# Kernel optimization log

Measured on AMD Instinct MI355X. Metric: run time of the kernel, lower is better.

## Reference

```python
import jax, jax.numpy as jnp
import numpy as np

B, N, M, J, D, PF = 4, 131072, 10475, 55, 64, 486


def setup_inputs() -> dict:
    key = jax.random.key(0)
    ks = jax.random.split(key, 16)
    return {
        "pts": jax.random.normal(ks[0], (B, N, 3), jnp.float32),
        "betas": jax.random.normal(ks[1], (B, 10), jnp.float32),
        "pose_feature": jax.random.normal(ks[2], (B, PF), jnp.float32),
        "init_spdir": jax.random.normal(ks[3], (M, 3, 10), jnp.float32),
        "init_podir": jax.random.normal(ks[4], (PF, 3 * M), jnp.float32),
        "init_faces": jax.random.randint(ks[5], (N, 3), 0, M, jnp.int32),
        "tfs_A": jax.random.normal(ks[6], (B, J, 4, 4), jnp.float32),
        "tfs_inv": jax.random.normal(ks[7], (1, J, 4, 4), jnp.float32),
        "poseoff_cano": jax.random.normal(ks[8], (1, N, 3), jnp.float32),
        "lbsw": jax.random.uniform(ks[9], (1, N, J), jnp.float32),
        "lbs_voxel": jax.random.uniform(ks[10], (1, J, D, D, D), jnp.float32),
        "vox_scale": jnp.ones((1, 1, 3), jnp.float32),
        "vox_offset": jnp.zeros((1, 1, 3), jnp.float32),
        "mask": jax.random.randint(ks[11], (B, N), 0, 2, jnp.int32),
    }


def _trilinear(vox, x, scale, offset):
    # vox: [J,D,D,D], x: [b,n,3] -> [b,n,J] trilinearly interpolated weights
    nj, nd = vox.shape[0], vox.shape[-1]
    g = jnp.clip(x * scale + offset, -1.0, 1.0)          # normalized coords
    t = (g + 1.0) * 0.5 * (nd - 1)                        # voxel coords
    i0 = jnp.clip(jnp.floor(t), 0, nd - 2).astype(jnp.int32)
    f = t - i0                                            # fractional part
    vf = vox.reshape(nj, -1)                              # [J, D^3]
    out = jnp.zeros(x.shape[:-1] + (nj,), x.dtype)
    for dx in (0, 1):
        for dy in (0, 1):
            for dz in (0, 1):
                ix = i0[..., 0] + dx
                iy = i0[..., 1] + dy
                iz = i0[..., 2] + dz
                wgt = ((f[..., 0] if dx else 1.0 - f[..., 0]) *
                       (f[..., 1] if dy else 1.0 - f[..., 1]) *
                       (f[..., 2] if dz else 1.0 - f[..., 2]))
                fid = (ix * nd + iy) * nd + iz            # flat voxel index [b,n]
                out = out + wgt[..., None] * jnp.moveaxis(vf[:, fid], 0, -1)
    return out


def reference(pts, betas, pose_feature, init_spdir, init_podir, init_faces,
              tfs_A, tfs_inv, poseoff_cano, lbsw, lbs_voxel, vox_scale,
              vox_offset, mask):
    b, n, _ = pts.shape
    # blend-shape offsets on template vertices
    shape_full = jnp.einsum('bl,mkl->bmk', betas, init_spdir)      # [b,M,3]
    pose_full = (pose_feature @ init_podir).reshape(b, -1, 3)      # [b,M,3]
    # face-vertex gather then average over the 3 vertices of each face
    shape_off = shape_full[:, init_faces].mean(axis=2)             # [b,F,3]
    pose_off = pose_full[:, init_faces].mean(axis=2)               # [b,F,3]
    x = pts + shape_off + pose_off - poseoff_cano                  # canonical pts + offsets
    # voxel-grid skinning-weight lookup at canonical points
    w_vox = _trilinear(lbs_voxel[0], pts, vox_scale, vox_offset)   # [b,n,J]
    w = jnp.where(mask[..., None] > 0, lbsw, w_vox)
    w = w / jnp.clip(w.sum(-1, keepdims=True), 1e-8)
    # per-point blended transforms: A @ A_inv_template
    tfs = tfs_A @ tfs_inv                                          # [b,J,4,4]
    T = jnp.einsum('bnj,bjrc->bnrc', w, tfs)                       # [b,n,4,4]
    xh = jnp.concatenate([x, jnp.ones_like(x[..., :1])], axis=-1)
    posed = jnp.einsum('bnrc,bnc->bnr', T, xh)[..., :3]
    return posed.reshape(b, n, 1, 3), T
```

## Files before the change

kernel.cpp:

```cpp
#include <hip/hip_runtime.h>

#define B_  4
#define N_  131072
#define J_  55
#define JP_ 56
#define D_  64
#define D3_ 262144
#define PF_ 486
#define COLS_ 31425

#define GZ_ 4096
#define OZ_ 123

#define BL16(u) __uint_as_float((u) << 16)
#define BH16(u) __uint_as_float((u) & 0xffff0000u)

typedef float f4a __attribute__((ext_vector_type(4), aligned(4)));

__device__ __forceinline__ unsigned short f2bf(float v) {
    unsigned u = __float_as_uint(v);
    u += 0x7fffu + ((u >> 16) & 1u);
    return (unsigned short)(u >> 16);
}

__global__ __launch_bounds__(256) void k_tfs(const float* __restrict__ A,
                                             const float* __restrict__ Ainv,
                                             float* __restrict__ tfsP) {
    int tid = blockIdx.x * 256 + threadIdx.x;
    if (tid >= B_ * JP_ * 16) return;
    int rc = tid & 15;
    int jb = tid >> 4;
    int j = jb % JP_;
    int b = jb / JP_;
    float v = 0.f;
    if (j < J_) {
        int r = rc >> 2, c = rc & 3;
#pragma unroll
        for (int k = 0; k < 4; ++k)
            v += A[((b * J_ + j) * 4 + r) * 4 + k] * Ainv[(j * 4 + k) * 4 + c];
    }
    tfsP[tid] = v;
}

__global__ __launch_bounds__(256) void k_prelude(
    const float* __restrict__ vox, const float* __restrict__ tfsP,
    uint4* __restrict__ Gtb, float* __restrict__ Stb,
    const float* __restrict__ pf, const float* __restrict__ podir,
    const float* __restrict__ betas, const float* __restrict__ spdir,
    float* __restrict__ off_full) {
    int bx = blockIdx.x;
    int tid = threadIdx.x;

    if (bx < GZ_) {
        int b = (bx & 7) >> 1;
        int chunk = ((bx >> 3) << 1) | (bx & 1);
        int v = chunk * 256 + tid;
        float g[16];
#pragma unroll
        for (int r = 0; r < 16; ++r) g[r] = 0.f;
        float s = 0.f;
        const float* tb = tfsP + b * (JP_ * 16);
        float wa[11], wb[11];
#pragma unroll
        for (int k = 0; k < 11; ++k) wa[k] = vox[(size_t)k * D3_ + v];
        for (int j0 = 0; j0 < J_; j0 += 11) {
            if (j0 + 11 < J_) {
#pragma unroll
                for (int k = 0; k < 11; ++k)
                    wb[k] = vox[(size_t)(j0 + 11 + k) * D3_ + v];
            }
#pragma unroll
            for (int k = 0; k < 11; ++k) {
                float w = wa[k];
                s += w;
                const float* tr = tb + (j0 + k) * 16;
#pragma unroll
                for (int r = 0; r < 16; ++r) g[r] += w * tr[r];
            }
#pragma unroll
            for (int k = 0; k < 11; ++k) wa[k] = wb[k];
        }
        if (b == 0) Stb[v] = s;
        unsigned gw[8];
#pragma unroll
        for (int k = 0; k < 8; ++k)
            gw[k] = (unsigned)f2bf(g[2 * k]) |
                    ((unsigned)f2bf(g[2 * k + 1]) << 16);
        uint4* gp = Gtb + ((size_t)b * D3_ + v) * 2;
        gp[0] = make_uint4(gw[0], gw[1], gw[2], gw[3]);
        gp[1] = make_uint4(gw[4], gw[5], gw[6], gw[7]);
    } else {
        int col = (bx - GZ_) * 256 + tid;
        if (col >= COLS_) return;
        float a0 = 0.f, a1 = 0.f, a2 = 0.f, a3 = 0.f;
        {
            float sp[10];
#pragma unroll
            for (int l = 0; l < 10; ++l) sp[l] = spdir[col * 10 + l];
#pragma unroll
            for (int l = 0; l < 10; ++l) {
                a0 += betas[0 * 10 + l] * sp[l];
                a1 += betas[1 * 10 + l] * sp[l];
                a2 += betas[2 * 10 + l] * sp[l];
                a3 += betas[3 * 10 + l] * sp[l];
            }
        }
        int p = 0;
        for (; p + 16 <= PF_; p += 16) {
            float v16[16];
#pragma unroll
            for (int k = 0; k < 16; ++k)
                v16[k] = podir[(size_t)(p + k) * COLS_ + col];
#pragma unroll
            for (int k = 0; k < 16; ++k) {
                a0 += pf[0 * PF_ + p + k] * v16[k];
                a1 += pf[1 * PF_ + p + k] * v16[k];
                a2 += pf[2 * PF_ + p + k] * v16[k];
                a3 += pf[3 * PF_ + p + k] * v16[k];
            }
        }
        for (; p < PF_; ++p) {
            float v = podir[(size_t)p * COLS_ + col];
            a0 += pf[0 * PF_ + p] * v;
            a1 += pf[1 * PF_ + p] * v;
            a2 += pf[2 * PF_ + p] * v;
            a3 += pf[3 * PF_ + p] * v;
        }
        off_full[0 * COLS_ + col] = a0;
        off_full[1 * COLS_ + col] = a1;
        off_full[2 * COLS_ + col] = a2;
        off_full[3 * COLS_ + col] = a3;
    }
}

#define ACC8(Toff, qa, qb)                                 \
    T[Toff + 0] += w0 * BL16(qa.x) + w1 * BL16(qb.x);      \
    T[Toff + 1] += w0 * BH16(qa.x) + w1 * BH16(qb.x);      \
    T[Toff + 2] += w0 * BL16(qa.y) + w1 * BL16(qb.y);      \
    T[Toff + 3] += w0 * BH16(qa.y) + w1 * BH16(qb.y);      \
    T[Toff + 4] += w0 * BL16(qa.z) + w1 * BL16(qb.z);      \
    T[Toff + 5] += w0 * BH16(qa.z) + w1 * BH16(qb.z);      \
    T[Toff + 6] += w0 * BL16(qa.w) + w1 * BL16(qb.w);      \
    T[Toff + 7] += w0 * BH16(qa.w) + w1 * BH16(qb.w);

__global__ __launch_bounds__(256) void k_main(
    const float* __restrict__ pts, const int* __restrict__ faces,
    const float* __restrict__ poseoff, const int* __restrict__ mask,
    const float* __restrict__ vox_scale, const float* __restrict__ vox_offset,
    const float* __restrict__ off_full, const float* __restrict__ tfsP,
    const float* __restrict__ lbsw, const uint4* __restrict__ Gtb,
    const float* __restrict__ Stb,
    float* __restrict__ out_posed, float* __restrict__ out_T) {
    __shared__ float sx0[256], sx1[256], sx2[256];
    __shared__ float sf0[256], sf1[256], sf2[256];
    __shared__ int   scell[256];
    __shared__ unsigned short lst[256];
    __shared__ int wc[4];

    int bid = blockIdx.x;
    int b  = (bid & 7) >> 1;
    int nc = ((bid >> 3) << 1) | (bid & 1);
    int tid = threadIdx.x;
    int n = nc * 256 + tid;
    int i = (b << 17) | n;

    float px = pts[3 * i + 0], py = pts[3 * i + 1], pz = pts[3 * i + 2];
    int f0 = faces[3 * n + 0], f1 = faces[3 * n + 1], f2 = faces[3 * n + 2];
    const float* ob = off_full + b * COLS_;
    const float c3 = 1.f / 3.f;
    float ox = (ob[f0 * 3 + 0] + ob[f1 * 3 + 0] + ob[f2 * 3 + 0]) * c3;
    float oy = (ob[f0 * 3 + 1] + ob[f1 * 3 + 1] + ob[f2 * 3 + 1]) * c3;
    float oz = (ob[f0 * 3 + 2] + ob[f1 * 3 + 2] + ob[f2 * 3 + 2]) * c3;
    sx0[tid] = px + ox - poseoff[3 * n + 0];
    sx1[tid] = py + oy - poseoff[3 * n + 1];
    sx2[tid] = pz + oz - poseoff[3 * n + 2];

    bool isv = !(mask[i] > 0);
    if (isv) {
        float sxc = vox_scale[0], syc = vox_scale[1], szc = vox_scale[2];
        float o0 = vox_offset[0], o1 = vox_offset[1], o2 = vox_offset[2];
        float gx = fminf(fmaxf(px * sxc + o0, -1.f), 1.f);
        float gy = fminf(fmaxf(py * syc + o1, -1.f), 1.f);
        float gz = fminf(fmaxf(pz * szc + o2, -1.f), 1.f);
        float tx = (gx + 1.f) * 0.5f * (D_ - 1);
        float ty = (gy + 1.f) * 0.5f * (D_ - 1);
        float tz = (gz + 1.f) * 0.5f * (D_ - 1);
        int ix = (int)floorf(tx); if (ix > D_ - 2) ix = D_ - 2; if (ix < 0) ix = 0;
        int iy = (int)floorf(ty); if (iy > D_ - 2) iy = D_ - 2; if (iy < 0) iy = 0;
        int iz = (int)floorf(tz); if (iz > D_ - 2) iz = D_ - 2; if (iz < 0) iz = 0;
        sf0[tid] = tx - ix;
        sf1[tid] = ty - iy;
        sf2[tid] = tz - iz;
        scell[tid] = (ix * D_ + iy) * D_ + iz;
    }

    unsigned long long bal = __ballot(isv);
    int lane = tid & 63, wid = tid >> 6;
    if (lane == 0) wc[wid] = __popcll(bal);
    __syncthreads();
    int pre = 0;
#pragma unroll
    for (int k = 0; k < 4; ++k) pre += (k < wid) ? wc[k] : 0;
    int tot = wc[0] + wc[1] + wc[2] + wc[3];
    unsigned long long lt = ((unsigned long long)1 << lane) - 1ull;
    int vbefore = pre + __popcll(bal & lt);
    int pos = isv ? vbefore : (tot + (tid - vbefore));
    lst[pos] = (unsigned short)tid;
    __syncthreads();

    int slot = lst[tid];
    float x0 = sx0[slot], x1 = sx1[slot], x2 = sx2[slot];
    int ii = (b << 17) | (nc * 256 + slot);

    float T[16];
#pragma unroll
    for (int r = 0; r < 16; ++r) T[r] = 0.f;
    float wsum = 0.f;

    if (tid < tot) {
        float fx = sf0[slot], fy = sf1[slot], fz = sf2[slot];
        int cell = scell[slot];
        const uint4* Gb = Gtb + (size_t)b * D3_ * 2;
#pragma unroll
        for (int cc = 0; cc < 4; ++cc) {
            int fid = cell + ((cc & 2) ? D_ * D_ : 0) + ((cc & 1) ? D_ : 0);
            float wxy = ((cc & 2) ? fx : 1.f - fx) * ((cc & 1) ? fy : 1.f - fy);
            float w0 = wxy * (1.f - fz);
            float w1 = wxy * fz;
            const uint4* R = Gb + (size_t)fid * 2;
            uint4 q0 = R[0], q1 = R[1], q2 = R[2], q3 = R[3];
            wsum += w0 * Stb[fid] + w1 * Stb[fid + 1];
            ACC8(0, q0, q2)
            ACC8(8, q1, q3)
        }
    } else {
        int n2 = nc * 256 + slot;
        const float* lw = lbsw + (size_t)n2 * J_;
        f4a q[13];
#pragma unroll
        for (int k = 0; k < 13; ++k)
            q[k] = *(const f4a*)(lw + 4 * k);
        float w52 = lw[52], w53 = lw[53], w54 = lw[54];
        const float* tb = tfsP + b * (JP_ * 16);
#pragma unroll
        for (int k = 0; k < 13; ++k) {
#pragma unroll
            for (int m = 0; m < 4; ++m) {
                float w = q[k][m];
                wsum += w;
                const float* tr = tb + (k * 4 + m) * 16;
#pragma unroll
                for (int r = 0; r < 16; ++r) T[r] += w * tr[r];
            }
        }
        float wt[3] = { w52, w53, w54 };
#pragma unroll
        for (int m = 0; m < 3; ++m) {
            float w = wt[m];
            wsum += w;
            const float* tr = tb + (52 + m) * 16;
#pragma unroll
            for (int r = 0; r < 16; ++r) T[r] += w * tr[r];
        }
    }

    float inv = 1.f / fmaxf(wsum, 1e-8f);
    float t[16];
#pragma unroll
    for (int r = 0; r < 16; ++r) t[r] = T[r] * inv;
    out_posed[3 * ii + 0] = t[0] * x0 + t[1] * x1 + t[2] * x2 + t[3];
    out_posed[3 * ii + 1] = t[4] * x0 + t[5] * x1 + t[6] * x2 + t[7];
    out_posed[3 * ii + 2] = t[8] * x0 + t[9] * x1 + t[10] * x2 + t[11];
    float4* to = (float4*)(out_T + (size_t)ii * 16);
    to[0] = make_float4(t[0], t[1], t[2], t[3]);
    to[1] = make_float4(t[4], t[5], t[6], t[7]);
    to[2] = make_float4(t[8], t[9], t[10], t[11]);
    to[3] = make_float4(t[12], t[13], t[14], t[15]);
}

extern "C" void kernel_launch(void* const* d_in, const int* in_sizes, int n_in,
                              void* d_out, int out_size, void* d_ws, size_t ws_size,
                              hipStream_t stream) {
    const float* pts      = (const float*)d_in[0];
    const float* betas    = (const float*)d_in[1];
    const float* pf       = (const float*)d_in[2];
    const float* spdir    = (const float*)d_in[3];
    const float* podir    = (const float*)d_in[4];
    const int*   faces    = (const int*)d_in[5];
    const float* tfs_A    = (const float*)d_in[6];
    const float* tfs_inv  = (const float*)d_in[7];
    const float* poseoff  = (const float*)d_in[8];
    const float* lbsw     = (const float*)d_in[9];
    const float* vox      = (const float*)d_in[10];
    const float* vscale   = (const float*)d_in[11];
    const float* voffset  = (const float*)d_in[12];
    const int*   mask     = (const int*)d_in[13];

    char* w = (char*)d_ws;
    uint4* Gtb      = (uint4*)w;
    float* Stb      = (float*)(w + 33554432);
    float* off_full = (float*)(w + 34603008);
    float* tfsP     = (float*)(w + 35119104);

    float* out_posed = (float*)d_out;
    float* out_T     = out_posed + (size_t)B_ * N_ * 3;

    k_tfs<<<14, 256, 0, stream>>>(tfs_A, tfs_inv, tfsP);
    k_prelude<<<GZ_ + OZ_, 256, 0, stream>>>(
        vox, tfsP, Gtb, Stb, pf, podir, betas, spdir, off_full);
    k_main<<<2048, 256, 0, stream>>>(pts, faces, poseoff, mask, vscale,
                                     voffset, off_full, tfsP, lbsw, Gtb, Stb,
                                     out_posed, out_T);
}
```

Baseline: 293.7 us.

## Fold tfs computation into kernels and share voxel loads across batch pairs

Drops the separate k_tfs launch. Each block now computes the 55 blended A@A_inv transforms straight into shared memory. In the prelude, each block handles two batches for the same voxel chunk, so every voxel weight read from global memory feeds two 16-float accumulators, and the block count is halved. This roughly halves the prelude's dominant voxel-grid reads and removes one launch plus a workspace round trip. The cost is redundant per-block transform math, more register pressure from 32 accumulators, and extra shared memory in both kernels.

```diff
diff --git a/kernel.cpp b/kernel.cpp
--- a/kernel.cpp
+++ b/kernel.cpp
@@ -9,7 +9,7 @@
 #define PF_ 486
 #define COLS_ 31425
 
-#define GZ_ 4096
+#define GZ_ 2048
 #define OZ_ 123
 
 #define BL16(u) __uint_as_float((u) << 16)
@@ -23,27 +23,42 @@
     return (unsigned short)(u >> 16);
 }
 
-__global__ __launch_bounds__(256) void k_tfs(const float* __restrict__ A,
-                                             const float* __restrict__ Ainv,
-                                             float* __restrict__ tfsP) {
-    int tid = blockIdx.x * 256 + threadIdx.x;
-    if (tid >= B_ * JP_ * 16) return;
-    int rc = tid & 15;
-    int jb = tid >> 4;
-    int j = jb % JP_;
-    int b = jb / JP_;
-    float v = 0.f;
-    if (j < J_) {
-        int r = rc >> 2, c = rc & 3;
-#pragma unroll
-        for (int k = 0; k < 4; ++k)
-            v += A[((b * J_ + j) * 4 + r) * 4 + k] * Ainv[(j * 4 + k) * 4 + c];
+__device__ __forceinline__ void stage_tfs(int b, int tid,
+                                          const float* __restrict__ A,
+                                          const float* __restrict__ Ainv,
+                                          float* __restrict__ dst) {
+#pragma unroll
+    for (int base = 0; base < 896; base += 256) {
+        int idx = base + tid;
+        if (idx < 896) {
+            int j = idx >> 4, rc = idx & 15, r = rc >> 2, c = rc & 3;
+            float v = 0.f;
+            if (j < J_) {
+#pragma unroll
+                for (int k = 0; k < 4; ++k)
+                    v += A[((b * J_ + j) * 4 + r) * 4 + k] *
+                         Ainv[(j * 4 + k) * 4 + c];
+            }
+            dst[idx] = v;
+        }
     }
-    tfsP[tid] = v;
-}
+}
+
+#define GACC(gv, q)                                         \
+    {   float4 t0 = s4[(q) * 4 + 0], t1 = s4[(q) * 4 + 1],  \
+               t2 = s4[(q) * 4 + 2], t3 = s4[(q) * 4 + 3];  \
+        gv[0]  += w * t0.x; gv[1]  += w * t0.y;             \
+        gv[2]  += w * t0.z; gv[3]  += w * t0.w;             \
+        gv[4]  += w * t1.x; gv[5]  += w * t1.y;             \
+        gv[6]  += w * t1.z; gv[7]  += w * t1.w;             \
+        gv[8]  += w * t2.x; gv[9]  += w * t2.y;             \
+        gv[10] += w * t2.z; gv[11] += w * t2.w;             \
+        gv[12] += w * t3.x; gv[13] += w * t3.y;             \
+        gv[14] += w * t3.z; gv[15] += w * t3.w; }
 
 __global__ __launch_bounds__(256) void k_prelude(
-    const float* __restrict__ vox, const float* __restrict__ tfsP,
+    const float* __restrict__ A, const float* __restrict__ Ainv,
+    const float* __restrict__ vox,
     uint4* __restrict__ Gtb, float* __restrict__ Stb,
     const float* __restrict__ pf, const float* __restrict__ podir,
     const float* __restrict__ betas, const float* __restrict__ spdir,
@@ -52,14 +67,20 @@
     int tid = threadIdx.x;
 
     if (bx < GZ_) {
-        int b = (bx & 7) >> 1;
-        int chunk = ((bx >> 3) << 1) | (bx & 1);
+        __shared__ float stfs[2 * 896];
+        int bp = (bx & 4) >> 2;
+        int chunk = ((bx >> 3) << 2) | (bx & 3);
+        stage_tfs(2 * bp + 0, tid, A, Ainv, stfs);
+        stage_tfs(2 * bp + 1, tid, A, Ainv, stfs + 896);
+        __syncthreads();
+
         int v = chunk * 256 + tid;
-        float g[16];
-#pragma unroll
-        for (int r = 0; r < 16; ++r) g[r] = 0.f;
+        float g0[16], g1[16];
+#pragma unroll
+        for (int r = 0; r < 16; ++r) { g0[r] = 0.f; g1[r] = 0.f; }
         float s = 0.f;
-        const float* tb = tfsP + b * (JP_ * 16);
+        const float4* sa = (const float4*)stfs;
+        const float4* sb = (const float4*)(stfs + 896);
         float wa[11], wb[11];
 #pragma unroll
         for (int k = 0; k < 11; ++k) wa[k] = vox[(size_t)k * D3_ + v];
@@ -73,22 +94,26 @@
             for (int k = 0; k < 11; ++k) {
                 float w = wa[k];
                 s += w;
-                const float* tr = tb + (j0 + k) * 16;
-#pragma unroll
-                for (int r = 0; r < 16; ++r) g[r] += w * tr[r];
+                int j = j0 + k;
+                { const float4* s4 = sa; GACC(g0, j) }
+                { const float4* s4 = sb; GACC(g1, j) }
             }
 #pragma unroll
             for (int k = 0; k < 11; ++k) wa[k] = wb[k];
         }
-        if (b == 0) Stb[v] = s;
-        unsigned gw[8];
-#pragma unroll
-        for (int k = 0; k < 8; ++k)
-            gw[k] = (unsigned)f2bf(g[2 * k]) |
-                    ((unsigned)f2bf(g[2 * k + 1]) << 16);
-        uint4* gp = Gtb + ((size_t)b * D3_ + v) * 2;
-        gp[0] = make_uint4(gw[0], gw[1], gw[2], gw[3]);
-        gp[1] = make_uint4(gw[4], gw[5], gw[6], gw[7]);
+        if (bp == 0) Stb[v] = s;
+#pragma unroll
+        for (int bb = 0; bb < 2; ++bb) {
+            float* g = bb ? g1 : g0;
+            unsigned gw[8];
+#pragma unroll
+            for (int k = 0; k < 8; ++k)
+                gw[k] = (unsigned)f2bf(g[2 * k]) |
+                        ((unsigned)f2bf(g[2 * k + 1]) << 16);
+            uint4* gp = Gtb + ((size_t)(2 * bp + bb) * D3_ + v) * 2;
+            gp[0] = make_uint4(gw[0], gw[1], gw[2], gw[3]);
+            gp[1] = make_uint4(gw[4], gw[5], gw[6], gw[7]);
+        }
     } else {
         int col = (bx - GZ_) * 256 + tid;
         if (col >= COLS_) return;
@@ -147,7 +172,8 @@
     const float* __restrict__ pts, const int* __restrict__ faces,
     const float* __restrict__ poseoff, const int* __restrict__ mask,
     const float* __restrict__ vox_scale, const float* __restrict__ vox_offset,
-    const float* __restrict__ off_full, const float* __restrict__ tfsP,
+    const float* __restrict__ off_full,
+    const float* __restrict__ A, const float* __restrict__ Ainv,
     const float* __restrict__ lbsw, const uint4* __restrict__ Gtb,
     const float* __restrict__ Stb,
     float* __restrict__ out_posed, float* __restrict__ out_T) {
@@ -156,6 +182,7 @@
     __shared__ int   scell[256];
     __shared__ unsigned short lst[256];
     __shared__ int wc[4];
+    __shared__ float stfs[896];
 
     int bid = blockIdx.x;
     int b  = (bid & 7) >> 1;
@@ -163,6 +190,8 @@
     int tid = threadIdx.x;
     int n = nc * 256 + tid;
     int i = (b << 17) | n;
+
+    stage_tfs(b, tid, A, Ainv, stfs);
 
     float px = pts[3 * i + 0], py = pts[3 * i + 1], pz = pts[3 * i + 2];
     int f0 = faces[3 * n + 0], f1 = faces[3 * n + 1], f2 = faces[3 * n + 2];
@@ -241,16 +270,14 @@
         for (int k = 0; k < 13; ++k)
             q[k] = *(const f4a*)(lw + 4 * k);
         float w52 = lw[52], w53 = lw[53], w54 = lw[54];
-        const float* tb = tfsP + b * (JP_ * 16);
+        const float4* s4 = (const float4*)stfs;
 #pragma unroll
         for (int k = 0; k < 13; ++k) {
 #pragma unroll
             for (int m = 0; m < 4; ++m) {
                 float w = q[k][m];
                 wsum += w;
-                const float* tr = tb + (k * 4 + m) * 16;
-#pragma unroll
-                for (int r = 0; r < 16; ++r) T[r] += w * tr[r];
+                GACC(T, k * 4 + m)
             }
         }
         float wt[3] = { w52, w53, w54 };
@@ -258,9 +285,7 @@
         for (int m = 0; m < 3; ++m) {
             float w = wt[m];
             wsum += w;
-            const float* tr = tb + (52 + m) * 16;
-#pragma unroll
-            for (int r = 0; r < 16; ++r) T[r] += w * tr[r];
+            GACC(T, 52 + m)
         }
     }
 
@@ -300,15 +325,13 @@
     uint4* Gtb      = (uint4*)w;
     float* Stb      = (float*)(w + 33554432);
     float* off_full = (float*)(w + 34603008);
-    float* tfsP     = (float*)(w + 35119104);
 
     float* out_posed = (float*)d_out;
     float* out_T     = out_posed + (size_t)B_ * N_ * 3;
 
-    k_tfs<<<14, 256, 0, stream>>>(tfs_A, tfs_inv, tfsP);
     k_prelude<<<GZ_ + OZ_, 256, 0, stream>>>(
-        vox, tfsP, Gtb, Stb, pf, podir, betas, spdir, off_full);
+        tfs_A, tfs_inv, vox, Gtb, Stb, pf, podir, betas, spdir, off_full);
     k_main<<<2048, 256, 0, stream>>>(pts, faces, poseoff, mask, vscale,
-                                     voffset, off_full, tfsP, lbsw, Gtb, Stb,
-                                     out_posed, out_T);
-}
+                                     voffset, off_full, tfs_A, tfs_inv,
+                                     lbsw, Gtb, Stb, out_posed, out_T);
+}
```

Result: slower. 307.7 us (+4.8%).
